# Optimization experiments

Measured on AMD Instinct MI355X. Metric: run time of the kernel, lower is better.

Reference implementation:

```python
import jax, jax.numpy as jnp
import numpy as np

DIM, H, DH, MLP, ADIM = 512, 8, 64, 2048, 256
B, T = 4, 2048
EPS = 1e-5


def setup_inputs() -> dict:
    key = jax.random.key(0)
    ks = jax.random.split(key, 10)
    s = 0.02
    inner = H * DH
    return {
        "x": jax.random.normal(ks[0], (B, T, DIM), jnp.float32),
        "action_emb": jax.random.normal(ks[1], (B, T, ADIM), jnp.float32),
        "causal_mask": jnp.tril(jnp.ones((T, T), dtype=bool)),
        "Wqkv": jax.random.normal(ks[2], (3 * inner, DIM), jnp.float32) * s,
        "Wout": jax.random.normal(ks[3], (DIM, inner), jnp.float32) * s,
        "bout": jnp.zeros((DIM,), jnp.float32),
        "W1": jax.random.normal(ks[4], (MLP, DIM), jnp.float32) * s,
        "b1": jnp.zeros((MLP,), jnp.float32),
        "W2": jax.random.normal(ks[5], (DIM, MLP), jnp.float32) * s,
        "b2": jnp.zeros((DIM,), jnp.float32),
        # adaLN is zero-init in the module; use small random so modulation is exercised
        "Wmod": jax.random.normal(ks[6], (6 * DIM, ADIM), jnp.float32) * s,
        "bmod": jnp.zeros((6 * DIM,), jnp.float32),
    }


def _layernorm(z):
    mu = jnp.mean(z, axis=-1, keepdims=True)
    var = jnp.var(z, axis=-1, keepdims=True)
    return (z - mu) * jax.lax.rsqrt(var + EPS)


def reference(x, action_emb, causal_mask, Wqkv, Wout, bout, W1, b1, W2, b2, Wmod, bmod):
    b, t, d = x.shape
    mod = jax.nn.silu(action_emb) @ Wmod.T + bmod            # (B,T,6*dim)
    shift1, scale1, gate1, shift2, scale2, gate2 = jnp.split(mod, 6, axis=-1)

    h = _layernorm(x) * (1.0 + scale1) + shift1
    qkv = (h @ Wqkv.T).reshape(b, t, 3, H, DH)
    q, k, v = qkv[:, :, 0], qkv[:, :, 1], qkv[:, :, 2]        # (B,T,H,DH)
    scores = jnp.einsum("bqhd,bkhd->bhqk", q, k) * (DH ** -0.5)
    scores = jnp.where(causal_mask, scores, -jnp.inf)
    attn = jax.nn.softmax(scores, axis=-1)                   # dropout=eval (identity)
    h = jnp.einsum("bhqk,bkhd->bqhd", attn, v).reshape(b, t, H * DH)
    h = h @ Wout.T + bout
    x = x + gate1 * h

    h = _layernorm(x) * (1.0 + scale2) + shift2
    h = jax.nn.gelu(h @ W1.T + b1, approximate=False) @ W2.T + b2
    return x + gate2 * h
```

## Files before the change

kernel.cpp:

```cpp
#include <hip/hip_runtime.h>
#include <math.h>
#include <stdint.h>

#define BB 4
#define TT 2048
#define NTOK 8192
#define DIMD 512
#define HH 8
#define DHH 64
#define MLPD 2048
#define ADIMD 256
#define MODD 3072
#define LNEPS 1e-5f
#define LOG2E_8 0.18033688011112042f

typedef short short8 __attribute__((ext_vector_type(8)));
typedef unsigned short ushort4v __attribute__((ext_vector_type(4)));
typedef __bf16 bf16x8 __attribute__((ext_vector_type(8)));
typedef float f32x4 __attribute__((ext_vector_type(4)));

static __device__ __forceinline__ unsigned short f2bf(float f) {
    union { float f; unsigned u; } v; v.f = f;
    unsigned r = v.u + 0x7fffu + ((v.u >> 16) & 1u);
    return (unsigned short)(r >> 16);
}
static __device__ __forceinline__ float bf2f(unsigned short u) {
    union { unsigned u; float f; } v; v.u = (unsigned)u << 16; return v.f;
}

static __device__ __forceinline__ f32x4 mfma_bf16(short8 a, short8 b, f32x4 c) {
    return __builtin_amdgcn_mfma_f32_16x16x32_bf16(
        __builtin_bit_cast(bf16x8, a), __builtin_bit_cast(bf16x8, b), c, 0, 0, 0);
}

static __device__ __forceinline__ void gld16(const void* g, const void* l) {
    __builtin_amdgcn_global_load_lds(
        (const __attribute__((address_space(1))) unsigned*)(unsigned long long)(uintptr_t)g,
        (__attribute__((address_space(3))) unsigned*)(unsigned)(uintptr_t)l,
        16, 0, 0);
}

struct CvtArgs {
    const float* s[6];
    unsigned short* d[6];
    int cum[7];
};
__global__ __launch_bounds__(256) void cvt_all(CvtArgs a)
{
    const int i = blockIdx.x * 256 + threadIdx.x;
    if (i >= a.cum[6]) return;
    int seg = 0;
    #pragma unroll
    for (int k = 1; k < 6; k++) seg += (i >= a.cum[k]);
    const int off = i - a.cum[seg];
    float4 v = ((const float4*)a.s[seg])[off];
    if (seg == 5) {
        v.x = v.x / (1.f + __expf(-v.x));
        v.y = v.y / (1.f + __expf(-v.y));
        v.z = v.z / (1.f + __expf(-v.z));
        v.w = v.w / (1.f + __expf(-v.w));
    }
    ushort4v o = { f2bf(v.x), f2bf(v.y), f2bf(v.z), f2bf(v.w) };
    ((ushort4v*)a.d[seg])[off] = o;
}

template<int EPI, int BN>
__global__ __launch_bounds__(256) void gemm_bf16(
    const unsigned short* __restrict__ A, const unsigned short* __restrict__ Bw,
    const float* __restrict__ bias, const float* __restrict__ res,
    const unsigned short* __restrict__ mod,
    int M, int N, int K,
    void* __restrict__ Cv)
{
    constexpr int MT = (BN == 128) ? 4 : 2;
    __shared__ unsigned short As[128 * 32];
    __shared__ unsigned short Bs[BN * 32];

    const int tid = threadIdx.x;
    const int w = tid >> 6, lane = tid & 63;
    const int quad = lane >> 4, l16 = lane & 15;
    const int wrow = (BN == 128) ? (w >> 1) * 64 : w * 32;
    const int wcol = (BN == 128) ? (w & 1) * 64 : 0;
    const int row0 = blockIdx.y * 128, col0 = blockIdx.x * BN;

    const int lrow = lane >> 2;
    const int lch  = (lane & 3) * 8;

    f32x4 acc[MT][4];
    #pragma unroll
    for (int i = 0; i < MT; i++)
        #pragma unroll
        for (int j = 0; j < 4; j++) acc[i][j] = (f32x4){0.f, 0.f, 0.f, 0.f};

    for (int k0 = 0; k0 < K; k0 += 32) {
        __syncthreads();
        #pragma unroll
        for (int c = 0; c < 2; c++) {
            const int r = w * 16 + c * 64;
            gld16(&A[(size_t)(row0 + r + lrow) * K + k0 + lch], &As[r * 32]);
            if (BN == 128)
                gld16(&Bw[(size_t)(col0 + r + lrow) * K + k0 + lch], &Bs[r * 32]);
        }
        if (BN == 64) {
            const int r = w * 16;
            gld16(&Bw[(size_t)(col0 + r + lrow) * K + k0 + lch], &Bs[r * 32]);
        }
        __syncthreads();

        short8 af[MT], bf[4];
        #pragma unroll
        for (int mt = 0; mt < MT; mt++)
            af[mt] = *(const short8*)&As[(wrow + mt * 16 + l16) * 32 + quad * 8];
        #pragma unroll
        for (int nt = 0; nt < 4; nt++)
            bf[nt] = *(const short8*)&Bs[(wcol + nt * 16 + l16) * 32 + quad * 8];
        #pragma unroll
        for (int nt = 0; nt < 4; nt++)
            #pragma unroll
            for (int mt = 0; mt < MT; mt++)
                acc[mt][nt] = mfma_bf16(af[mt], bf[nt], acc[mt][nt]);
    }

    float* Cf = (float*)Cv;
    unsigned short* Cb = (unsigned short*)Cv;
    #pragma unroll
    for (int mt = 0; mt < MT; mt++) {
        #pragma unroll
        for (int r = 0; r < 4; r++) {
            const int row = row0 + wrow + mt * 16 + quad * 4 + r;
            #pragma unroll
            for (int nt = 0; nt < 4; nt++) {
                const int col = col0 + wcol + nt * 16 + l16;
                const size_t idx = (size_t)row * N + col;
                const float v = acc[mt][nt][r];
                if (EPI == 0) {
                    Cb[idx] = f2bf(v);
                } else if (EPI == 2) {
                    float t = v + bias[col];
                    Cb[idx] = f2bf(0.5f * t * (1.f + erff(t * 0.70710678118654752f)));
                } else if (EPI == 3) {
                    float t = v + bias[col];
                    Cf[idx] = res[idx] + bf2f(mod[(size_t)row * MODD + 1024 + col]) * t;
                } else if (EPI == 4) {
                    float t = v + bias[col];
                    Cf[idx] = Cf[idx] + bf2f(mod[(size_t)row * MODD + 2560 + col]) * t;
                } else if (EPI == 5) {
                    Cb[idx] = f2bf(v + bias[col]);
                }
            }
        }
    }
}

__global__ __launch_bounds__(256) void adaln_ln(
    const float* __restrict__ src, const unsigned short* __restrict__ mod,
    unsigned short* __restrict__ dst, int shift_off, int scale_off)
{
    const int n = blockIdx.x;
    const int tid = threadIdx.x;
    const float* xr = src + (size_t)n * DIMD;
    float v0 = xr[tid], v1 = xr[tid + 256];
    float s = v0 + v1;
    float q = v0 * v0 + v1 * v1;
    #pragma unroll
    for (int o = 32; o > 0; o >>= 1) {
        s += __shfl_down(s, o);
        q += __shfl_down(q, o);
    }
    __shared__ float sh[8];
    __shared__ float mu_sh, rs_sh;
    const int wid = tid >> 6, lane = tid & 63;
    if (lane == 0) { sh[wid] = s; sh[wid + 4] = q; }
    __syncthreads();
    if (tid == 0) {
        float S = sh[0] + sh[1] + sh[2] + sh[3];
        float Q = sh[4] + sh[5] + sh[6] + sh[7];
        float mu = S * (1.f / DIMD);
        float var = Q * (1.f / DIMD) - mu * mu;
        mu_sh = mu;
        rs_sh = rsqrtf(var + LNEPS);
    }
    __syncthreads();
    const float mu = mu_sh, rs = rs_sh;
    const unsigned short* mrow = mod + (size_t)n * MODD;
    const size_t o0 = (size_t)n * DIMD + tid;
    dst[o0]       = f2bf((v0 - mu) * rs * (1.f + bf2f(mrow[scale_off + tid]))       + bf2f(mrow[shift_off + tid]));
    dst[o0 + 256] = f2bf((v1 - mu) * rs * (1.f + bf2f(mrow[scale_off + tid + 256])) + bf2f(mrow[shift_off + tid + 256]));
}

__global__ __launch_bounds__(256, 2) void attn_mfma(
    const unsigned short* __restrict__ qkv, unsigned short* __restrict__ outb)
{
    __shared__ unsigned short Kt[128][72];
    __shared__ unsigned short Vt[64][136];
    __shared__ unsigned short Ps[4][32][136];

    const int qi = (TT / 128 - 1) - blockIdx.x;
    const int h = blockIdx.y, b = blockIdx.z;
    const int tid = threadIdx.x;
    const int w = tid >> 6;
    const int lane = tid & 63;
    const int quad = lane >> 4;
    const int l16 = lane & 15;

    const int qw = qi * 128 + w * 32;
    const size_t tokbase = (size_t)b * TT;

    short8 qf[2][2];
    #pragma unroll
    for (int nt = 0; nt < 2; nt++) {
        const unsigned short* qp = qkv + (tokbase + qw + nt * 16 + l16) * 1536 + h * 64 + quad * 8;
        #pragma unroll
        for (int hd = 0; hd < 2; hd++) {
            short8 raw = *(const short8*)(qp + hd * 32);
            short8 f;
            #pragma unroll
            for (int j = 0; j < 8; j++)
                f[j] = (short)f2bf(bf2f((unsigned short)raw[j]) * LOG2E_8);
            qf[nt][hd] = f;
        }
    }

    f32x4 Oa[4][2];
    float mrun[2] = {-INFINITY, -INFINITY}, lrun[2] = {0.f, 0.f};
    #pragma unroll
    for (int mt = 0; mt < 4; mt++)
        #pragma unroll
        for (int nt = 0; nt < 2; nt++) Oa[mt][nt] = (f32x4){0.f, 0.f, 0.f, 0.f};

    const int nkt = qi + 1;
    const int vk0 = (tid & 63) * 2;
    const int vdb = (tid >> 6) * 8;

    short8 kpre[4], vpre[4];
    auto prefetchKV = [&](int kt) {
        const unsigned short* kb = qkv + (tokbase + (size_t)kt * 128) * 1536 + 512 + h * 64;
        #pragma unroll
        for (int it = 0; it < 4; it++) {
            const int i = tid + it * 256;
            kpre[it] = *(const short8*)(kb + (size_t)(i >> 3) * 1536 + (i & 7) * 8);
        }
        const unsigned short* vb = qkv + (tokbase + (size_t)kt * 128 + vk0) * 1536 + 1024 + h * 64;
        #pragma unroll
        for (int p = 0; p < 2; p++) {
            vpre[2 * p]     = *(const short8*)(vb + p * 32 + vdb);
            vpre[2 * p + 1] = *(const short8*)(vb + 1536 + p * 32 + vdb);
        }
    };
    auto storeKV = [&]() {
        #pragma unroll
        for (int it = 0; it < 4; it++) {
            const int i = tid + it * 256;
            *(short8*)&Kt[i >> 3][(i & 7) * 8] = kpre[it];
        }
        #pragma unroll
        for (int p = 0; p < 2; p++)
            #pragma unroll
            for (int j = 0; j < 8; j++) {
                const int d = p * 32 + vdb + j;
                *(unsigned*)&Vt[d][vk0] =
                    (unsigned)(unsigned short)vpre[2 * p][j]
                    | ((unsigned)(unsigned short)vpre[2 * p + 1][j] << 16);
            }
    };

    prefetchKV(0);
    storeKV();
    __syncthreads();

    for (int kt = 0; kt < nkt; kt++) {
        const bool haveNext = (kt + 1 < nkt);
        if (haveNext) prefetchKV(kt + 1);

        short8 af[8][2];
        #pragma unroll
        for (int mk = 0; mk < 8; mk++) {
            af[mk][0] = *(const short8*)&Kt[mk * 16 + l16][quad * 8];
            af[mk][1] = *(const short8*)&Kt[mk * 16 + l16][32 + quad * 8];
        }
        #pragma unroll
        for (int nt = 0; nt < 2; nt++) {
            f32x4 st[8];
            #pragma unroll
            for (int mk = 0; mk < 8; mk++) {
                st[mk] = (f32x4){0.f, 0.f, 0.f, 0.f};
                st[mk] = mfma_bf16(af[mk][0], qf[nt][0], st[mk]);
                st[mk] = mfma_bf16(af[mk][1], qf[nt][1], st[mk]);
            }
            if (kt == qi) {
                const int qrel = w * 32 + nt * 16 + l16;
                #pragma unroll
                for (int mk = 0; mk < 8; mk++)
                    #pragma unroll
                    for (int r = 0; r < 4; r++)
                        if (mk * 16 + quad * 4 + r > qrel) st[mk][r] = -INFINITY;
            }
            float tm = -INFINITY;
            #pragma unroll
            for (int mk = 0; mk < 8; mk++)
                #pragma unroll
                for (int r = 0; r < 4; r++) tm = fmaxf(tm, st[mk][r]);
            tm = fmaxf(tm, __shfl_xor(tm, 16));
            tm = fmaxf(tm, __shfl_xor(tm, 32));
            const float mn = fmaxf(mrun[nt], tm);
            const float alpha = __builtin_amdgcn_exp2f(mrun[nt] - mn);
            mrun[nt] = mn;
            float ts = 0.f;
            #pragma unroll
            for (int mk = 0; mk < 8; mk++) {
                const float p0 = __builtin_amdgcn_exp2f(st[mk][0] - mn);
                const float p1 = __builtin_amdgcn_exp2f(st[mk][1] - mn);
                const float p2 = __builtin_amdgcn_exp2f(st[mk][2] - mn);
                const float p3 = __builtin_amdgcn_exp2f(st[mk][3] - mn);
                ts += (p0 + p1) + (p2 + p3);
                const unsigned long long pk =
                    (unsigned long long)f2bf(p0)
                    | ((unsigned long long)f2bf(p1) << 16)
                    | ((unsigned long long)f2bf(p2) << 32)
                    | ((unsigned long long)f2bf(p3) << 48);
                *(unsigned long long*)&Ps[w][nt * 16 + l16][mk * 16 + quad * 4] = pk;
            }
            ts += __shfl_xor(ts, 16);
            ts += __shfl_xor(ts, 32);
            lrun[nt] = lrun[nt] * alpha + ts;
            #pragma unroll
            for (int mt = 0; mt < 4; mt++) Oa[mt][nt] *= alpha;
        }
        __threadfence_block();

        short8 pf0[4], pf1[4];
        #pragma unroll
        for (int kc = 0; kc < 4; kc++) {
            pf0[kc] = *(const short8*)&Ps[w][l16][kc * 32 + quad * 8];
            pf1[kc] = *(const short8*)&Ps[w][16 + l16][kc * 32 + quad * 8];
        }
        #pragma unroll
        for (int mt = 0; mt < 4; mt++)
            #pragma unroll
            for (int kc = 0; kc < 4; kc++) {
                const short8 vf = *(const short8*)&Vt[mt * 16 + l16][kc * 32 + quad * 8];
                Oa[mt][0] = mfma_bf16(vf, pf0[kc], Oa[mt][0]);
                Oa[mt][1] = mfma_bf16(vf, pf1[kc], Oa[mt][1]);
            }

        __syncthreads();
        if (haveNext) storeKV();
        __syncthreads();
    }

    #pragma unroll
    for (int nt = 0; nt < 2; nt++) {
        const float inv = 1.f / lrun[nt];
        const size_t tok = tokbase + qw + nt * 16 + l16;
        #pragma unroll
        for (int mt = 0; mt < 4; mt++) {
            const unsigned long long pk =
                (unsigned long long)f2bf(Oa[mt][nt][0] * inv)
                | ((unsigned long long)f2bf(Oa[mt][nt][1] * inv) << 16)
                | ((unsigned long long)f2bf(Oa[mt][nt][2] * inv) << 32)
                | ((unsigned long long)f2bf(Oa[mt][nt][3] * inv) << 48);
            *(unsigned long long*)&outb[tok * DIMD + h * 64 + mt * 16 + quad * 4] = pk;
        }
    }
}

extern "C" void kernel_launch(void* const* d_in, const int* in_sizes, int n_in,
                              void* d_out, int out_size, void* d_ws, size_t ws_size,
                              hipStream_t stream)
{
    (void)in_sizes; (void)n_in; (void)out_size; (void)ws_size;

    const float* x    = (const float*)d_in[0];
    const float* aemb = (const float*)d_in[1];
    const float* Wqkv = (const float*)d_in[3];
    const float* Wout = (const float*)d_in[4];
    const float* bout = (const float*)d_in[5];
    const float* W1   = (const float*)d_in[6];
    const float* b1   = (const float*)d_in[7];
    const float* W2   = (const float*)d_in[8];
    const float* b2   = (const float*)d_in[9];
    const float* Wmod = (const float*)d_in[10];
    const float* bmod = (const float*)d_in[11];

    float* out = (float*)d_out;

    char* p = (char*)d_ws;
    unsigned short* modw = (unsigned short*)p; p += (size_t)NTOK * MODD * 2;
    unsigned short* h12  = (unsigned short*)p; p += (size_t)NTOK * DIMD * 2;
    unsigned short* qkvb = (unsigned short*)p; p += (size_t)NTOK * 1536 * 2;
    unsigned short* attw = (unsigned short*)p; p += (size_t)NTOK * DIMD * 2;
    unsigned short* hid  = qkvb;
    unsigned short* sact = (unsigned short*)p; p += (size_t)NTOK * ADIMD * 2;
    unsigned short* wq = (unsigned short*)p;   p += (size_t)1536 * 512 * 2;
    unsigned short* wo = (unsigned short*)p;   p += (size_t)512 * 512 * 2;
    unsigned short* w1 = (unsigned short*)p;   p += (size_t)2048 * 512 * 2;
    unsigned short* w2 = (unsigned short*)p;   p += (size_t)512 * 2048 * 2;
    unsigned short* wm = (unsigned short*)p;   p += (size_t)3072 * 256 * 2;

    CvtArgs ca;
    ca.s[0] = Wqkv; ca.d[0] = wq;
    ca.s[1] = Wout; ca.d[1] = wo;
    ca.s[2] = W1;   ca.d[2] = w1;
    ca.s[3] = W2;   ca.d[3] = w2;
    ca.s[4] = Wmod; ca.d[4] = wm;
    ca.s[5] = aemb; ca.d[5] = sact;
    const int n4s[6] = {1536 * 512 / 4, 512 * 512 / 4, 2048 * 512 / 4,
                        512 * 2048 / 4, 3072 * 256 / 4, NTOK * ADIMD / 4};
    ca.cum[0] = 0;
    for (int i = 0; i < 6; i++) ca.cum[i + 1] = ca.cum[i] + n4s[i];
    cvt_all<<<(ca.cum[6] + 255) / 256, 256, 0, stream>>>(ca);

    gemm_bf16<5, 128><<<dim3(MODD / 128, NTOK / 128), 256, 0, stream>>>(
        sact, wm, bmod, nullptr, nullptr, NTOK, MODD, ADIMD, modw);

    adaln_ln<<<NTOK, 256, 0, stream>>>(x, modw, h12, 0, 512);

    gemm_bf16<0, 128><<<dim3(1536 / 128, NTOK / 128), 256, 0, stream>>>(
        h12, wq, nullptr, nullptr, nullptr, NTOK, 1536, DIMD, qkvb);

    attn_mfma<<<dim3(TT / 128, HH, BB), 256, 0, stream>>>(qkvb, attw);

    gemm_bf16<3, 64><<<dim3(DIMD / 64, NTOK / 128), 256, 0, stream>>>(
        attw, wo, bout, x, modw, NTOK, DIMD, DIMD, out);

    adaln_ln<<<NTOK, 256, 0, stream>>>(out, modw, h12, 1536, 2048);

    gemm_bf16<2, 128><<<dim3(MLPD / 128, NTOK / 128), 256, 0, stream>>>(
        h12, w1, b1, nullptr, nullptr, NTOK, MLPD, DIMD, hid);

    gemm_bf16<4, 64><<<dim3(DIMD / 64, NTOK / 128), 256, 0, stream>>>(
        hid, w2, b2, nullptr, modw, NTOK, DIMD, MLPD, out);
}
```

Measured before the change: 352.5 us.

## Register-prefetch GEMM tiles with BK=64 and padded LDS rows

Replaces the direct global-to-LDS loads in the bf16 GEMM with register prefetch. The next K-tile is loaded into registers while MFMAs run on the current tile, then written to LDS after a barrier. The K step grows from 32 to 64, and LDS rows are padded to 72 elements to avoid bank conflicts on the fragment reads. The aim is to hide global load latency and halve the barrier count per K. The cost is more VGPRs (prefetch buffers) and more LDS per block, which may reduce occupancy.

```diff
diff --git a/kernel.cpp b/kernel.cpp
--- a/kernel.cpp
+++ b/kernel.cpp
@@ -33,13 +33,6 @@
         __builtin_bit_cast(bf16x8, a), __builtin_bit_cast(bf16x8, b), c, 0, 0, 0);
 }
 
-static __device__ __forceinline__ void gld16(const void* g, const void* l) {
-    __builtin_amdgcn_global_load_lds(
-        (const __attribute__((address_space(1))) unsigned*)(unsigned long long)(uintptr_t)g,
-        (__attribute__((address_space(3))) unsigned*)(unsigned)(uintptr_t)l,
-        16, 0, 0);
-}
-
 struct CvtArgs {
     const float* s[6];
     unsigned short* d[6];
@@ -73,8 +66,9 @@
     void* __restrict__ Cv)
 {
     constexpr int MT = (BN == 128) ? 4 : 2;
-    __shared__ unsigned short As[128 * 32];
-    __shared__ unsigned short Bs[BN * 32];
+    constexpr int NPB = (BN == 128) ? 4 : 2;
+    __shared__ unsigned short As[128 * 72];
+    __shared__ unsigned short Bs[BN * 72];
 
     const int tid = threadIdx.x;
     const int w = tid >> 6, lane = tid & 63;
@@ -83,8 +77,8 @@
     const int wcol = (BN == 128) ? (w & 1) * 64 : 0;
     const int row0 = blockIdx.y * 128, col0 = blockIdx.x * BN;
 
-    const int lrow = lane >> 2;
-    const int lch  = (lane & 3) * 8;
+    const int srow = tid >> 3;
+    const int skc  = (tid & 7) * 8;
 
     f32x4 acc[MT][4];
     #pragma unroll
@@ -92,33 +86,50 @@
         #pragma unroll
         for (int j = 0; j < 4; j++) acc[i][j] = (f32x4){0.f, 0.f, 0.f, 0.f};
 
-    for (int k0 = 0; k0 < K; k0 += 32) {
+    short8 pA[4], pB[NPB];
+    auto prefetch = [&](int k0) {
+        #pragma unroll
+        for (int p = 0; p < 4; p++)
+            pA[p] = *(const short8*)&A[(size_t)(row0 + srow + p * 32) * K + k0 + skc];
+        #pragma unroll
+        for (int p = 0; p < NPB; p++)
+            pB[p] = *(const short8*)&Bw[(size_t)(col0 + srow + p * 32) * K + k0 + skc];
+    };
+    auto stage = [&]() {
+        #pragma unroll
+        for (int p = 0; p < 4; p++)
+            *(short8*)&As[(srow + p * 32) * 72 + skc] = pA[p];
+        #pragma unroll
+        for (int p = 0; p < NPB; p++)
+            *(short8*)&Bs[(srow + p * 32) * 72 + skc] = pB[p];
+    };
+
+    prefetch(0);
+    stage();
+    __syncthreads();
+
+    for (int k0 = 0; k0 < K; k0 += 64) {
+        const bool more = (k0 + 64 < K);
+        if (more) prefetch(k0 + 64);
+
+        #pragma unroll
+        for (int ks = 0; ks < 2; ks++) {
+            short8 af[MT], bf[4];
+            #pragma unroll
+            for (int mt = 0; mt < MT; mt++)
+                af[mt] = *(const short8*)&As[(wrow + mt * 16 + l16) * 72 + ks * 32 + quad * 8];
+            #pragma unroll
+            for (int nt = 0; nt < 4; nt++)
+                bf[nt] = *(const short8*)&Bs[(wcol + nt * 16 + l16) * 72 + ks * 32 + quad * 8];
+            #pragma unroll
+            for (int nt = 0; nt < 4; nt++)
+                #pragma unroll
+                for (int mt = 0; mt < MT; mt++)
+                    acc[mt][nt] = mfma_bf16(af[mt], bf[nt], acc[mt][nt]);
+        }
         __syncthreads();
-        #pragma unroll
-        for (int c = 0; c < 2; c++) {
-            const int r = w * 16 + c * 64;
-            gld16(&A[(size_t)(row0 + r + lrow) * K + k0 + lch], &As[r * 32]);
-            if (BN == 128)
-                gld16(&Bw[(size_t)(col0 + r + lrow) * K + k0 + lch], &Bs[r * 32]);
-        }
-        if (BN == 64) {
-            const int r = w * 16;
-            gld16(&Bw[(size_t)(col0 + r + lrow) * K + k0 + lch], &Bs[r * 32]);
-        }
+        if (more) stage();
         __syncthreads();
-
-        short8 af[MT], bf[4];
-        #pragma unroll
-        for (int mt = 0; mt < MT; mt++)
-            af[mt] = *(const short8*)&As[(wrow + mt * 16 + l16) * 32 + quad * 8];
-        #pragma unroll
-        for (int nt = 0; nt < 4; nt++)
-            bf[nt] = *(const short8*)&Bs[(wcol + nt * 16 + l16) * 32 + quad * 8];
-        #pragma unroll
-        for (int nt = 0; nt < 4; nt++)
-            #pragma unroll
-            for (int mt = 0; mt < MT; mt++)
-                acc[mt][nt] = mfma_bf16(af[mt], bf[nt], acc[mt][nt]);
     }
 
     float* Cf = (float*)Cv;
```

New measurement: 338.1 us. 1.04x faster.
